# Kernel tuning notes

Measured on AMD Instinct MI355X. Metric: run time of the kernel, lower is better.

## Reference

```python
import jax, jax.numpy as jnp
import numpy as np

N_NODES = 50000
N_EDGES = 600000
N_FEAT = 128
N_DIMS = 128
N_CLSS = 10


def setup_inputs() -> dict:
    key = jax.random.key(0)
    ks = jax.random.split(key, 9)
    x = jax.random.normal(ks[0], (N_NODES, N_FEAT), dtype=jnp.float32)
    edge_index = jax.random.randint(ks[1], (2, N_EDGES), 0, N_NODES, dtype=jnp.int32)
    edge_weight = jax.random.uniform(ks[2], (N_EDGES,), dtype=jnp.float32)
    # Glorot-ish init for learned params
    W1 = jax.random.normal(ks[3], (N_FEAT, N_DIMS), dtype=jnp.float32) * (1.0 / np.sqrt(N_FEAT))
    b1 = jnp.zeros((N_DIMS,), dtype=jnp.float32)
    W2 = jax.random.normal(ks[4], (N_DIMS, N_DIMS), dtype=jnp.float32) * (1.0 / np.sqrt(N_DIMS))
    b2 = jnp.zeros((N_DIMS,), dtype=jnp.float32)
    Wc = jax.random.normal(ks[5], (N_DIMS, N_CLSS), dtype=jnp.float32) * (1.0 / np.sqrt(N_DIMS))
    bc = jnp.zeros((N_CLSS,), dtype=jnp.float32)
    return {"x": x, "edge_index": edge_index, "edge_weight": edge_weight,
            "W1": W1, "b1": b1, "W2": W2, "b2": b2, "Wc": Wc, "bc": bc}


def gcn_conv(x, W, b, src, dst, ew, n_nodes):
    """PyG GCNConv (add_self_loops=True, improved=False, bias=True).
    out[i] = sum_{(j->i) in E} d_i^-1/2 * w_ji * d_j^-1/2 * (xW)[j]
             + d_i^-1 * (xW)[i]  (self loop, weight 1) + b
    where d_i = 1 + sum of incoming edge weights at i.
    """
    h = x @ W                                                   # [N, D]
    deg = jax.ops.segment_sum(ew, dst, num_segments=n_nodes) + 1.0  # self-loop weight 1
    dinv = jax.lax.rsqrt(deg)                                   # deg >= 1, no inf
    norm = dinv[src] * ew * dinv[dst]                           # [E]
    agg = jax.ops.segment_sum(h[src] * norm[:, None], dst, num_segments=n_nodes)
    agg = agg + h * (dinv * dinv)[:, None]                      # self-loop term
    return agg + b


def reference(x, edge_index, edge_weight, W1, b1, W2, b2, Wc, bc):
    n = x.shape[0]
    src, dst = edge_index[0], edge_index[1]
    h = jax.nn.relu(gcn_conv(x, W1, b1, src, dst, edge_weight, n))
    # dropout is identity in eval mode
    h = gcn_conv(h, W2, b2, src, dst, edge_weight, n)
    h = jax.nn.relu(h)
    return h @ Wc + bc
```

## Files before the change

kernel.cpp:

```cpp
#include <hip/hip_runtime.h>
#include <hip/hip_bf16.h>

#define N_NODES 50000
#define N_EDGES 600000
#define NC 10
#define GB ((N_NODES + 63) / 64)

typedef __attribute__((ext_vector_type(8))) __bf16 bf16x8;
typedef __attribute__((ext_vector_type(8))) unsigned short u16x8;
typedef __attribute__((ext_vector_type(4))) float f32x4;

__device__ __forceinline__ unsigned short f2bf(float f) {
    unsigned u = __float_as_uint(f);
    u += 0x7fff + ((u >> 16) & 1);
    return (unsigned short)(u >> 16);
}
__device__ __forceinline__ int rfl(int x) { return __builtin_amdgcn_readfirstlane(x); }
__device__ __forceinline__ float rflf(float x) {
    return __uint_as_float(__builtin_amdgcn_readfirstlane(__float_as_uint(x)));
}

__global__ void k_zero(int4* __restrict__ p, int n4) {
    int i = blockIdx.x * blockDim.x + threadIdx.x;
    if (i < n4) p[i] = make_int4(0, 0, 0, 0);
}

__global__ void k_prep(const float* __restrict__ W1, const float* __restrict__ W2,
                       unsigned short* __restrict__ wt1, unsigned short* __restrict__ wt2,
                       const int4* __restrict__ dst4, int* __restrict__ cnt,
                       int4* __restrict__ ord4) {
    int b = blockIdx.x;
    if (b < 128) {
        const float* W = (b < 64) ? W1 : W2;
        unsigned short* Wt = (b < 64) ? wt1 : wt2;
        int i = (b & 63) * 256 + threadIdx.x;
        int n = i >> 7, k = i & 127;
        Wt[n * 128 + k] = f2bf(W[k * 128 + n]);
    } else {
        int i = (b - 128) * 256 + threadIdx.x;
        if (i < N_EDGES / 4) {
            int4 d = dst4[i];
            int4 o;
            o.x = atomicAdd(&cnt[d.x], 1);
            o.y = atomicAdd(&cnt[d.y], 1);
            o.z = atomicAdd(&cnt[d.z], 1);
            o.w = atomicAdd(&cnt[d.w], 1);
            ord4[i] = o;
        }
    }
}

__global__ void k_scan1(const int* __restrict__ cnt, int* __restrict__ rowptr,
                        int* __restrict__ bsum, int n) {
    __shared__ int sh[256];
    int t = threadIdx.x;
    int i = blockIdx.x * 256 + t;
    int v = (i < n) ? cnt[i] : 0;
    sh[t] = v;
    __syncthreads();
    for (int off = 1; off < 256; off <<= 1) {
        int x = 0;
        if (t >= off) x = sh[t - off];
        __syncthreads();
        sh[t] += x;
        __syncthreads();
    }
    if (i < n) rowptr[i] = sh[t] - v;
    if (t == 255) bsum[blockIdx.x] = sh[255];
}

__global__ void k_scan2(int* __restrict__ bsum, int nb) {
    __shared__ int sh[256];
    int t = threadIdx.x;
    int v = (t < nb) ? bsum[t] : 0;
    sh[t] = v;
    __syncthreads();
    for (int off = 1; off < 256; off <<= 1) {
        int x = 0;
        if (t >= off) x = sh[t - off];
        __syncthreads();
        sh[t] += x;
        __syncthreads();
    }
    if (t < nb) bsum[t] = sh[t] - v;
}

__global__ void k_scan3(int* __restrict__ rowptr, const int* __restrict__ bsum, int n) {
    int t = threadIdx.x;
    int i = blockIdx.x * 256 + t;
    if (i < n) rowptr[i] += bsum[blockIdx.x];
    if (blockIdx.x == 0 && t == 0) rowptr[n] = N_EDGES;
}

template <int FP32IN>
__device__ __forceinline__ void gemm_body(unsigned short* Al, unsigned short* Bl,
                                          const void* __restrict__ Xin,
                                          const unsigned short* __restrict__ Wt,
                                          unsigned short* __restrict__ Yb,
                                          int M, int row0) {
    int t = threadIdx.x;
    for (int i = t; i < 2048; i += 256) {
        int r = i >> 4, q = i & 15;
        *(u16x8*)(Bl + r * 128 + ((q ^ (r & 7)) << 3)) =
            *(const u16x8*)(Wt + r * 128 + (q << 3));
    }
    for (int i = t; i < 1024; i += 256) {
        int r = i >> 4, q = i & 15;
        int gr = row0 + r;
        u16x8 v;
        if (FP32IN) {
            const float* X = (const float*)Xin;
            if (gr < M) {
                float4 f0 = *(const float4*)(X + (size_t)gr * 128 + (q << 3));
                float4 f1 = *(const float4*)(X + (size_t)gr * 128 + (q << 3) + 4);
                v[0] = f2bf(f0.x); v[1] = f2bf(f0.y); v[2] = f2bf(f0.z); v[3] = f2bf(f0.w);
                v[4] = f2bf(f1.x); v[5] = f2bf(f1.y); v[6] = f2bf(f1.z); v[7] = f2bf(f1.w);
            } else {
#pragma unroll
                for (int j = 0; j < 8; ++j) v[j] = 0;
            }
        } else {
            const unsigned short* X = (const unsigned short*)Xin;
            if (gr < M) {
                v = *(const u16x8*)(X + (size_t)gr * 128 + (q << 3));
            } else {
#pragma unroll
                for (int j = 0; j < 8; ++j) v[j] = 0;
            }
        }
        *(u16x8*)(Al + r * 128 + ((q ^ (r & 7)) << 3)) = v;
    }
    __syncthreads();

    int l  = t & 63;
    int w  = t >> 6;
    int ar = (w << 4) + (l & 15);
    int kq = l >> 4;

    bf16x8 af[4];
#pragma unroll
    for (int s = 0; s < 4; ++s) {
        int g = ((s << 2) + kq) ^ (l & 7);
        af[s] = *(const bf16x8*)(Al + ar * 128 + (g << 3));
    }

    f32x4 acc[8];
#pragma unroll
    for (int c = 0; c < 8; ++c)
#pragma unroll
        for (int j = 0; j < 4; ++j) acc[c][j] = 0.0f;

#pragma unroll
    for (int c = 0; c < 8; ++c) {
        int br = (c << 4) + (l & 15);
#pragma unroll
        for (int s = 0; s < 4; ++s) {
            int g = ((s << 2) + kq) ^ (l & 7);
            bf16x8 bf = *(const bf16x8*)(Bl + br * 128 + (g << 3));
            acc[c] = __builtin_amdgcn_mfma_f32_16x16x32_bf16(af[s], bf, acc[c], 0, 0, 0);
        }
    }

    int orow = row0 + (w << 4) + ((l >> 4) << 2);
    int ocol = l & 15;
#pragma unroll
    for (int c = 0; c < 8; ++c) {
#pragma unroll
        for (int j = 0; j < 4; ++j) {
            int r = orow + j;
            if (r < M) Yb[(size_t)r * 128 + (c << 4) + ocol] = f2bf(acc[c][j]);
        }
    }
}

__global__ __launch_bounds__(256) void k_sg(const float* __restrict__ X,
                                            const unsigned short* __restrict__ Wt,
                                            unsigned short* __restrict__ Yb, int M,
                                            const int* __restrict__ src,
                                            const int* __restrict__ dst,
                                            const float* __restrict__ ew,
                                            const int* __restrict__ ord,
                                            const int* __restrict__ rowptr,
                                            int* __restrict__ esrc,
                                            float* __restrict__ ew2) {
    __shared__ unsigned short Al[64 * 128];
    __shared__ unsigned short Bl[128 * 128];
    if (blockIdx.x < GB) {
        gemm_body<1>(Al, Bl, X, Wt, Yb, M, blockIdx.x * 64);
    } else {
        int e = (blockIdx.x - GB) * 256 + threadIdx.x;
        if (e < N_EDGES) {
            int pos = rowptr[dst[e]] + ord[e];
            esrc[pos] = src[e];
            ew2[pos]  = ew[e];
        }
    }
}

__global__ __launch_bounds__(256) void k_gemm_mfma(const unsigned short* __restrict__ Xb,
                                                   const unsigned short* __restrict__ Wt,
                                                   unsigned short* __restrict__ Yb, int M) {
    __shared__ unsigned short Al[64 * 128];
    __shared__ unsigned short Bl[128 * 128];
    gemm_body<0>(Al, Bl, Xb, Wt, Yb, M, blockIdx.x * 64);
}

__global__ void k_deg(const int* __restrict__ rowptr, const float* __restrict__ ew2,
                      float* __restrict__ dinv) {
    int i = blockIdx.x * blockDim.x + threadIdx.x;
    if (i >= N_NODES) return;
    int p1 = rowptr[i + 1];
    float s = 1.0f;
    for (int p = rowptr[i]; p < p1; ++p) s += ew2[p];
    dinv[i] = rsqrtf(s);
}

__global__ void k_norm(const int* __restrict__ rowptr, const int* __restrict__ esrc,
                       const float* __restrict__ ew2, const float* __restrict__ dinv,
                       float* __restrict__ enorm) {
    int i = blockIdx.x * blockDim.x + threadIdx.x;
    if (i >= N_NODES) return;
    float di = dinv[i];
    int p  = rowptr[i];
    int p1 = rowptr[i + 1];
    for (; p + 4 <= p1; p += 4) {
        int s0 = esrc[p], s1 = esrc[p+1], s2 = esrc[p+2], s3 = esrc[p+3];
        float d0 = dinv[s0], d1 = dinv[s1], d2 = dinv[s2], d3 = dinv[s3];
        enorm[p]   = d0 * ew2[p]   * di;
        enorm[p+1] = d1 * ew2[p+1] * di;
        enorm[p+2] = d2 * ew2[p+2] * di;
        enorm[p+3] = d3 * ew2[p+3] * di;
    }
    for (; p < p1; ++p) enorm[p] = dinv[esrc[p]] * ew2[p] * di;
}

template <int MODE>
__global__ __launch_bounds__(256) void k_agg(const unsigned* __restrict__ hb,
                                             const int* __restrict__ rowptr,
                                             const int* __restrict__ esrc,
                                             const float* __restrict__ enorm,
                                             const float* __restrict__ dinv,
                                             const float* __restrict__ bias,
                                             const float* __restrict__ Wc,
                                             const float* __restrict__ bc,
                                             float* __restrict__ out) {
    int wid  = (blockIdx.x * blockDim.x + threadIdx.x) >> 6;
    int lane = threadIdx.x & 63;
    if (wid >= N_NODES) return;
    wid = rfl(wid);
    int p  = rfl(rowptr[wid]);
    int p1 = rfl(rowptr[wid + 1]);
    float di  = dinv[wid];
    float di2 = di * di;
    unsigned sv = hb[(size_t)wid * 64 + lane];
    float2 acc;
    acc.x = __uint_as_float(sv << 16) * di2;
    acc.y = __uint_as_float(sv & 0xffff0000u) * di2;

    while (p + 16 <= p1) {
        int s[16]; float w[16]; unsigned v[16];
#pragma unroll
        for (int i = 0; i < 16; ++i) {
            s[i] = rfl(esrc[p + i]);
            w[i] = rflf(enorm[p + i]);
        }
#pragma unroll
        for (int i = 0; i < 16; ++i) v[i] = hb[(size_t)s[i] * 64 + lane];
#pragma unroll
        for (int i = 0; i < 16; ++i) {
            acc.x += w[i] * __uint_as_float(v[i] << 16);
            acc.y += w[i] * __uint_as_float(v[i] & 0xffff0000u);
        }
        p += 16;
    }
    while (p + 4 <= p1) {
        int s[4]; float w[4]; unsigned v[4];
#pragma unroll
        for (int i = 0; i < 4; ++i) {
            s[i] = rfl(esrc[p + i]);
            w[i] = rflf(enorm[p + i]);
        }
#pragma unroll
        for (int i = 0; i < 4; ++i) v[i] = hb[(size_t)s[i] * 64 + lane];
#pragma unroll
        for (int i = 0; i < 4; ++i) {
            acc.x += w[i] * __uint_as_float(v[i] << 16);
            acc.y += w[i] * __uint_as_float(v[i] & 0xffff0000u);
        }
        p += 4;
    }
    for (; p < p1; ++p) {
        int s = rfl(esrc[p]);
        float w = rflf(enorm[p]);
        unsigned v = hb[(size_t)s * 64 + lane];
        acc.x += w * __uint_as_float(v << 16);
        acc.y += w * __uint_as_float(v & 0xffff0000u);
    }

    float2 bv = ((const float2*)bias)[lane];
    acc.x = fmaxf(acc.x + bv.x, 0.f);
    acc.y = fmaxf(acc.y + bv.y, 0.f);
    if (MODE == 0) {
        unsigned lo = f2bf(acc.x), hi = f2bf(acc.y);
        ((unsigned*)out)[(size_t)wid * 64 + lane] = lo | (hi << 16);
    } else {
        int k0 = 2 * lane;
        float r[NC];
#pragma unroll
        for (int c = 0; c < NC; ++c)
            r[c] = acc.x * Wc[k0 * NC + c] + acc.y * Wc[(k0 + 1) * NC + c];
#pragma unroll
        for (int off = 32; off; off >>= 1)
#pragma unroll
            for (int c = 0; c < NC; ++c)
                r[c] += __shfl_xor(r[c], off, 64);
        if (lane < NC) out[(size_t)wid * NC + lane] = r[lane] + bc[lane];
    }
}

extern "C" void kernel_launch(void* const* d_in, const int* in_sizes, int n_in,
                              void* d_out, int out_size, void* d_ws, size_t ws_size,
                              hipStream_t stream) {
    const float* x   = (const float*)d_in[0];
    const int*   ei  = (const int*)d_in[1];
    const float* ew  = (const float*)d_in[2];
    const float* W1  = (const float*)d_in[3];
    const float* b1  = (const float*)d_in[4];
    const float* W2  = (const float*)d_in[5];
    const float* b2  = (const float*)d_in[6];
    const float* Wc  = (const float*)d_in[7];
    const float* bc  = (const float*)d_in[8];
    float*       out = (float*)d_out;

    const int* src = ei;
    const int* dst = ei + N_EDGES;

    size_t off = 0;
    auto carve = [&](size_t bytes) {
        void* p = (char*)d_ws + off;
        off += (bytes + 255) & ~(size_t)255;
        return p;
    };
    unsigned short* hb  = (unsigned short*)carve((size_t)N_NODES * 128 * 2);
    unsigned short* hb1 = (unsigned short*)carve((size_t)N_NODES * 128 * 2);
    unsigned short* wt1 = (unsigned short*)carve(128 * 128 * 2);
    unsigned short* wt2 = (unsigned short*)carve(128 * 128 * 2);
    float* dinv   = (float*)carve((size_t)N_NODES * 4);
    int*   cnt    = (int*)carve((size_t)N_NODES * 4);
    int*   rowptr = (int*)carve((size_t)(N_NODES + 1) * 4);
    int*   bsum   = (int*)carve(256 * 4);
    int*   ord    = (int*)carve((size_t)N_EDGES * 4);
    int*   esrc   = (int*)carve((size_t)N_EDGES * 4);
    float* ew2    = (float*)carve((size_t)N_EDGES * 4);
    float* enorm  = (float*)carve((size_t)N_EDGES * 4);
    (void)ws_size; (void)n_in; (void)in_sizes; (void)out_size;

    int nb = (N_NODES + 255) / 256;
    int eb = (N_EDGES + 255) / 256;

    k_zero<<<(N_NODES / 4 + 255) / 256, 256, 0, stream>>>((int4*)cnt, N_NODES / 4);
    k_prep<<<128 + (N_EDGES / 4 + 255) / 256, 256, 0, stream>>>(
        W1, W2, wt1, wt2, (const int4*)dst, cnt, (int4*)ord);
    k_scan1<<<nb, 256, 0, stream>>>(cnt, rowptr, bsum, N_NODES);
    k_scan2<<<1, 256, 0, stream>>>(bsum, nb);
    k_scan3<<<nb, 256, 0, stream>>>(rowptr, bsum, N_NODES);
    k_sg<<<GB + eb, 256, 0, stream>>>(x, wt1, hb, N_NODES,
                                      src, dst, ew, ord, rowptr, esrc, ew2);
    k_deg<<<nb, 256, 0, stream>>>(rowptr, ew2, dinv);
    k_norm<<<nb, 256, 0, stream>>>(rowptr, esrc, ew2, dinv, enorm);

    k_agg<0><<<(N_NODES + 3) / 4, 256, 0, stream>>>((const unsigned*)hb, rowptr, esrc,
                                                    enorm, dinv, b1, Wc, bc, (float*)hb1);
    k_gemm_mfma<<<GB, 256, 0, stream>>>(hb1, wt2, hb, N_NODES);
    k_agg<1><<<(N_NODES + 3) / 4, 256, 0, stream>>>((const unsigned*)hb, rowptr, esrc,
                                                    enorm, dinv, b2, Wc, bc, out);
}
```

Before: 157.9 us.

## Split wavefront into four edge groups with 16-byte row gathers in aggregation

Reworks the aggregation kernel so each 64-lane wave handles four edges at once. Each 16-lane group loads a full 256-byte bf16 row with uint4 loads instead of one dword per lane. The self-loop is folded in as an extra edge item, and partial sums are reduced across groups with shuffles. This aims for wider memory transactions and more gathers in flight per wave, at the cost of padding waste on low-degree nodes, select logic per step, and extra cross-lane reductions.

```diff
diff --git a/kernel.cpp b/kernel.cpp
--- a/kernel.cpp
+++ b/kernel.cpp
@@ -235,7 +235,7 @@
 }
 
 template <int MODE>
-__global__ __launch_bounds__(256) void k_agg(const unsigned* __restrict__ hb,
+__global__ __launch_bounds__(256) void k_agg(const unsigned short* __restrict__ hb,
                                              const int* __restrict__ rowptr,
                                              const int* __restrict__ esrc,
                                              const float* __restrict__ enorm,
@@ -248,72 +248,111 @@
     int lane = threadIdx.x & 63;
     if (wid >= N_NODES) return;
     wid = rfl(wid);
-    int p  = rfl(rowptr[wid]);
-    int p1 = rfl(rowptr[wid + 1]);
-    float di  = dinv[wid];
+    int p0  = rfl(rowptr[wid]);
+    int cnt = rfl(rowptr[wid + 1]) - p0;
+    float di  = rflf(dinv[wid]);
     float di2 = di * di;
-    unsigned sv = hb[(size_t)wid * 64 + lane];
-    float2 acc;
-    acc.x = __uint_as_float(sv << 16) * di2;
-    acc.y = __uint_as_float(sv & 0xffff0000u) * di2;
-
-    while (p + 16 <= p1) {
-        int s[16]; float w[16]; unsigned v[16];
-#pragma unroll
-        for (int i = 0; i < 16; ++i) {
-            s[i] = rfl(esrc[p + i]);
-            w[i] = rflf(enorm[p + i]);
-        }
-#pragma unroll
-        for (int i = 0; i < 16; ++i) v[i] = hb[(size_t)s[i] * 64 + lane];
-#pragma unroll
-        for (int i = 0; i < 16; ++i) {
-            acc.x += w[i] * __uint_as_float(v[i] << 16);
-            acc.y += w[i] * __uint_as_float(v[i] & 0xffff0000u);
-        }
-        p += 16;
-    }
-    while (p + 4 <= p1) {
-        int s[4]; float w[4]; unsigned v[4];
-#pragma unroll
-        for (int i = 0; i < 4; ++i) {
-            s[i] = rfl(esrc[p + i]);
-            w[i] = rflf(enorm[p + i]);
-        }
-#pragma unroll
-        for (int i = 0; i < 4; ++i) v[i] = hb[(size_t)s[i] * 64 + lane];
-#pragma unroll
-        for (int i = 0; i < 4; ++i) {
-            acc.x += w[i] * __uint_as_float(v[i] << 16);
-            acc.y += w[i] * __uint_as_float(v[i] & 0xffff0000u);
-        }
-        p += 4;
-    }
-    for (; p < p1; ++p) {
-        int s = rfl(esrc[p]);
-        float w = rflf(enorm[p]);
-        unsigned v = hb[(size_t)s * 64 + lane];
-        acc.x += w * __uint_as_float(v << 16);
-        acc.y += w * __uint_as_float(v & 0xffff0000u);
-    }
-
-    float2 bv = ((const float2*)bias)[lane];
-    acc.x = fmaxf(acc.x + bv.x, 0.f);
-    acc.y = fmaxf(acc.y + bv.y, 0.f);
+    int g = lane >> 4;
+    int q = lane & 15;
+
+    bool g0 = (g == 0), g1 = (g == 1), g2 = (g == 2);
+
+    float acc[8];
+#pragma unroll
+    for (int j = 0; j < 8; ++j) acc[j] = 0.f;
+
+    int items = cnt + 1;
+    int base = 0;
+
+#define STEP_META(B, SS, WW)                                                    \
+    {                                                                           \
+        int i0 = p0 + (B);                                                      \
+        int e0 = min(i0,     N_EDGES - 1), e1 = min(i0 + 1, N_EDGES - 1);       \
+        int e2 = min(i0 + 2, N_EDGES - 1), e3 = min(i0 + 3, N_EDGES - 1);       \
+        int   s0 = rfl(esrc[e0]),  s1 = rfl(esrc[e1]);                          \
+        int   s2 = rfl(esrc[e2]),  s3 = rfl(esrc[e3]);                          \
+        float w0 = rflf(enorm[e0]), w1 = rflf(enorm[e1]);                       \
+        float w2 = rflf(enorm[e2]), w3 = rflf(enorm[e3]);                       \
+        if ((B) >= cnt)     { s0 = wid; w0 = ((B) == cnt)     ? di2 : 0.f; }    \
+        if ((B) + 1 >= cnt) { s1 = wid; w1 = ((B) + 1 == cnt) ? di2 : 0.f; }    \
+        if ((B) + 2 >= cnt) { s2 = wid; w2 = ((B) + 2 == cnt) ? di2 : 0.f; }    \
+        if ((B) + 3 >= cnt) { s3 = wid; w3 = ((B) + 3 == cnt) ? di2 : 0.f; }    \
+        SS = g0 ? s0 : (g1 ? s1 : (g2 ? s2 : s3));                              \
+        WW = g0 ? w0 : (g1 ? w1 : (g2 ? w2 : w3));                              \
+    }
+
+#define STEP_ACC(WW, V)                                                         \
+    acc[0] += (WW) * __uint_as_float((V).x << 16);                              \
+    acc[1] += (WW) * __uint_as_float((V).x & 0xffff0000u);                      \
+    acc[2] += (WW) * __uint_as_float((V).y << 16);                              \
+    acc[3] += (WW) * __uint_as_float((V).y & 0xffff0000u);                      \
+    acc[4] += (WW) * __uint_as_float((V).z << 16);                              \
+    acc[5] += (WW) * __uint_as_float((V).z & 0xffff0000u);                      \
+    acc[6] += (WW) * __uint_as_float((V).w << 16);                              \
+    acc[7] += (WW) * __uint_as_float((V).w & 0xffff0000u);
+
+    while (base + 16 <= items) {
+        int   ss[4];
+        float ws[4];
+        uint4 vs[4];
+        STEP_META(base + 0,  ss[0], ws[0])
+        STEP_META(base + 4,  ss[1], ws[1])
+        STEP_META(base + 8,  ss[2], ws[2])
+        STEP_META(base + 12, ss[3], ws[3])
+#pragma unroll
+        for (int s = 0; s < 4; ++s)
+            vs[s] = *(const uint4*)(hb + (size_t)ss[s] * 128 + (q << 3));
+#pragma unroll
+        for (int s = 0; s < 4; ++s) { STEP_ACC(ws[s], vs[s]) }
+        base += 16;
+    }
+    while (base < items) {
+        int ssel; float wsel;
+        STEP_META(base, ssel, wsel)
+        uint4 v = *(const uint4*)(hb + (size_t)ssel * 128 + (q << 3));
+        STEP_ACC(wsel, v)
+        base += 4;
+    }
+#undef STEP_META
+#undef STEP_ACC
+
+#pragma unroll
+    for (int j = 0; j < 8; ++j) {
+        acc[j] += __shfl_xor(acc[j], 32, 64);
+        acc[j] += __shfl_xor(acc[j], 16, 64);
+    }
+
+    float4 b0 = *(const float4*)(bias + (q << 3));
+    float4 b1v = *(const float4*)(bias + (q << 3) + 4);
+    acc[0] = fmaxf(acc[0] + b0.x, 0.f);  acc[1] = fmaxf(acc[1] + b0.y, 0.f);
+    acc[2] = fmaxf(acc[2] + b0.z, 0.f);  acc[3] = fmaxf(acc[3] + b0.w, 0.f);
+    acc[4] = fmaxf(acc[4] + b1v.x, 0.f); acc[5] = fmaxf(acc[5] + b1v.y, 0.f);
+    acc[6] = fmaxf(acc[6] + b1v.z, 0.f); acc[7] = fmaxf(acc[7] + b1v.w, 0.f);
+
     if (MODE == 0) {
-        unsigned lo = f2bf(acc.x), hi = f2bf(acc.y);
-        ((unsigned*)out)[(size_t)wid * 64 + lane] = lo | (hi << 16);
+        if (lane < 16) {
+            uint4 ov;
+            ov.x = f2bf(acc[0]) | ((unsigned)f2bf(acc[1]) << 16);
+            ov.y = f2bf(acc[2]) | ((unsigned)f2bf(acc[3]) << 16);
+            ov.z = f2bf(acc[4]) | ((unsigned)f2bf(acc[5]) << 16);
+            ov.w = f2bf(acc[6]) | ((unsigned)f2bf(acc[7]) << 16);
+            *(uint4*)((unsigned short*)out + (size_t)wid * 128 + (q << 3)) = ov;
+        }
     } else {
-        int k0 = 2 * lane;
         float r[NC];
 #pragma unroll
-        for (int c = 0; c < NC; ++c)
-            r[c] = acc.x * Wc[k0 * NC + c] + acc.y * Wc[(k0 + 1) * NC + c];
-#pragma unroll
-        for (int off = 32; off; off >>= 1)
-#pragma unroll
-            for (int c = 0; c < NC; ++c)
-                r[c] += __shfl_xor(r[c], off, 64);
+        for (int c = 0; c < NC; ++c) r[c] = 0.f;
+#pragma unroll
+        for (int j = 0; j < 8; ++j) {
+            float a = acc[j];
+            const float* wrow = Wc + ((q << 3) + j) * NC;
+#pragma unroll
+            for (int c = 0; c < NC; ++c) r[c] += a * wrow[c];
+        }
+#pragma unroll
+        for (int off = 8; off; off >>= 1)
+#pragma unroll
+            for (int c = 0; c < NC; ++c) r[c] += __shfl_xor(r[c], off, 64);
         if (lane < NC) out[(size_t)wid * NC + lane] = r[lane] + bc[lane];
     }
 }
@@ -369,9 +408,9 @@
     k_deg<<<nb, 256, 0, stream>>>(rowptr, ew2, dinv);
     k_norm<<<nb, 256, 0, stream>>>(rowptr, esrc, ew2, dinv, enorm);
 
-    k_agg<0><<<(N_NODES + 3) / 4, 256, 0, stream>>>((const unsigned*)hb, rowptr, esrc,
+    k_agg<0><<<(N_NODES + 3) / 4, 256, 0, stream>>>(hb, rowptr, esrc,
                                                     enorm, dinv, b1, Wc, bc, (float*)hb1);
     k_gemm_mfma<<<GB, 256, 0, stream>>>(hb1, wt2, hb, N_NODES);
-    k_agg<1><<<(N_NODES + 3) / 4, 256, 0, stream>>>((const unsigned*)hb, rowptr, esrc,
+    k_agg<1><<<(N_NODES + 3) / 4, 256, 0, stream>>>(hb, rowptr, esrc,
                                                     enorm, dinv, b2, Wc, bc, out);
 }
```

Result: slower. 195.9 us (+24.0%).

## Fuse layer-1 aggregation with layer-2 GEMM via shared-memory tile

Applied to the files above, without the earlier changes.

Replaces the separate layer-1 aggregation kernel and the layer-2 MFMA GEMM with one kernel. Each 256-thread block aggregates 64 nodes (16 per wave) into a swizzled LDS tile, then multiplies that tile by W2 with MFMA and writes bf16 output. This drops one launch and the global round trip of the intermediate activations. In exchange, aggregation parallelism falls to 4 waves per 64 nodes with sequential per-wave loops, so latency hiding on the gather may suffer, and B fragments are read straight from global memory.

```diff
diff --git a/kernel.cpp b/kernel.cpp
--- a/kernel.cpp
+++ b/kernel.cpp
@@ -197,14 +197,6 @@
     }
 }
 
-__global__ __launch_bounds__(256) void k_gemm_mfma(const unsigned short* __restrict__ Xb,
-                                                   const unsigned short* __restrict__ Wt,
-                                                   unsigned short* __restrict__ Yb, int M) {
-    __shared__ unsigned short Al[64 * 128];
-    __shared__ unsigned short Bl[128 * 128];
-    gemm_body<0>(Al, Bl, Xb, Wt, Yb, M, blockIdx.x * 64);
-}
-
 __global__ void k_deg(const int* __restrict__ rowptr, const float* __restrict__ ew2,
                       float* __restrict__ dinv) {
     int i = blockIdx.x * blockDim.x + threadIdx.x;
@@ -234,7 +226,130 @@
     for (; p < p1; ++p) enorm[p] = dinv[esrc[p]] * ew2[p] * di;
 }
 
-template <int MODE>
+__device__ __forceinline__ float2 agg_row(const unsigned* __restrict__ hb,
+                                          const int* __restrict__ rowptr,
+                                          const int* __restrict__ esrc,
+                                          const float* __restrict__ enorm,
+                                          const float* __restrict__ dinv,
+                                          int node, int lane) {
+    int p  = rfl(rowptr[node]);
+    int p1 = rfl(rowptr[node + 1]);
+    float di  = dinv[node];
+    float di2 = di * di;
+    unsigned sv = hb[(size_t)node * 64 + lane];
+    float2 acc;
+    acc.x = __uint_as_float(sv << 16) * di2;
+    acc.y = __uint_as_float(sv & 0xffff0000u) * di2;
+
+    while (p + 16 <= p1) {
+        int s[16]; float w[16]; unsigned v[16];
+#pragma unroll
+        for (int i = 0; i < 16; ++i) {
+            s[i] = rfl(esrc[p + i]);
+            w[i] = rflf(enorm[p + i]);
+        }
+#pragma unroll
+        for (int i = 0; i < 16; ++i) v[i] = hb[(size_t)s[i] * 64 + lane];
+#pragma unroll
+        for (int i = 0; i < 16; ++i) {
+            acc.x += w[i] * __uint_as_float(v[i] << 16);
+            acc.y += w[i] * __uint_as_float(v[i] & 0xffff0000u);
+        }
+        p += 16;
+    }
+    while (p + 4 <= p1) {
+        int s[4]; float w[4]; unsigned v[4];
+#pragma unroll
+        for (int i = 0; i < 4; ++i) {
+            s[i] = rfl(esrc[p + i]);
+            w[i] = rflf(enorm[p + i]);
+        }
+#pragma unroll
+        for (int i = 0; i < 4; ++i) v[i] = hb[(size_t)s[i] * 64 + lane];
+#pragma unroll
+        for (int i = 0; i < 4; ++i) {
+            acc.x += w[i] * __uint_as_float(v[i] << 16);
+            acc.y += w[i] * __uint_as_float(v[i] & 0xffff0000u);
+        }
+        p += 4;
+    }
+    for (; p < p1; ++p) {
+        int s = rfl(esrc[p]);
+        float w = rflf(enorm[p]);
+        unsigned v = hb[(size_t)s * 64 + lane];
+        acc.x += w * __uint_as_float(v << 16);
+        acc.y += w * __uint_as_float(v & 0xffff0000u);
+    }
+    return acc;
+}
+
+__global__ __launch_bounds__(256) void k_ag(const unsigned* __restrict__ hb,
+                                            const int* __restrict__ rowptr,
+                                            const int* __restrict__ esrc,
+                                            const float* __restrict__ enorm,
+                                            const float* __restrict__ dinv,
+                                            const float* __restrict__ bias,
+                                            const unsigned short* __restrict__ Wt,
+                                            unsigned short* __restrict__ Yb, int M) {
+    __shared__ unsigned short Al[64 * 128];
+    int t = threadIdx.x;
+    int l = t & 63;
+    int w = t >> 6;
+    int row0 = blockIdx.x * 64;
+
+    for (int nd = 0; nd < 16; ++nd) {
+        int r = (w << 4) + nd;
+        int node = row0 + r;
+        float2 acc = make_float2(0.f, 0.f);
+        if (node < M) {
+            acc = agg_row(hb, rowptr, esrc, enorm, dinv, node, l);
+            float2 bv = ((const float2*)bias)[l];
+            acc.x = fmaxf(acc.x + bv.x, 0.f);
+            acc.y = fmaxf(acc.y + bv.y, 0.f);
+        }
+        unsigned val = f2bf(acc.x) | ((unsigned)f2bf(acc.y) << 16);
+        int q = l >> 2;
+        *(unsigned*)(Al + r * 128 + ((q ^ (r & 7)) << 3) + ((l & 3) << 1)) = val;
+    }
+    __syncthreads();
+
+    int ar = (w << 4) + (l & 15);
+    int kq = l >> 4;
+    bf16x8 af[4];
+#pragma unroll
+    for (int s = 0; s < 4; ++s) {
+        int g = ((s << 2) + kq) ^ (ar & 7);
+        af[s] = *(const bf16x8*)(Al + ar * 128 + (g << 3));
+    }
+
+    f32x4 acc2[8];
+#pragma unroll
+    for (int c = 0; c < 8; ++c)
+#pragma unroll
+        for (int j = 0; j < 4; ++j) acc2[c][j] = 0.0f;
+
+#pragma unroll
+    for (int c = 0; c < 8; ++c) {
+        int br = (c << 4) + (l & 15);
+#pragma unroll
+        for (int s = 0; s < 4; ++s) {
+            bf16x8 bf = *(const bf16x8*)(Wt + br * 128 + (((s << 2) + kq) << 3));
+            acc2[c] = __builtin_amdgcn_mfma_f32_16x16x32_bf16(af[s], bf, acc2[c], 0, 0, 0);
+        }
+    }
+
+    int orow = row0 + (w << 4) + ((l >> 4) << 2);
+    int ocol = l & 15;
+#pragma unroll
+    for (int c = 0; c < 8; ++c) {
+#pragma unroll
+        for (int j = 0; j < 4; ++j) {
+            int r = orow + j;
+            if (r < M) Yb[(size_t)r * 128 + (c << 4) + ocol] = f2bf(acc2[c][j]);
+        }
+    }
+}
+
 __global__ __launch_bounds__(256) void k_agg(const unsigned* __restrict__ hb,
                                              const int* __restrict__ rowptr,
                                              const int* __restrict__ esrc,
@@ -248,74 +363,22 @@
     int lane = threadIdx.x & 63;
     if (wid >= N_NODES) return;
     wid = rfl(wid);
-    int p  = rfl(rowptr[wid]);
-    int p1 = rfl(rowptr[wid + 1]);
-    float di  = dinv[wid];
-    float di2 = di * di;
-    unsigned sv = hb[(size_t)wid * 64 + lane];
-    float2 acc;
-    acc.x = __uint_as_float(sv << 16) * di2;
-    acc.y = __uint_as_float(sv & 0xffff0000u) * di2;
-
-    while (p + 16 <= p1) {
-        int s[16]; float w[16]; unsigned v[16];
-#pragma unroll
-        for (int i = 0; i < 16; ++i) {
-            s[i] = rfl(esrc[p + i]);
-            w[i] = rflf(enorm[p + i]);
-        }
-#pragma unroll
-        for (int i = 0; i < 16; ++i) v[i] = hb[(size_t)s[i] * 64 + lane];
-#pragma unroll
-        for (int i = 0; i < 16; ++i) {
-            acc.x += w[i] * __uint_as_float(v[i] << 16);
-            acc.y += w[i] * __uint_as_float(v[i] & 0xffff0000u);
-        }
-        p += 16;
-    }
-    while (p + 4 <= p1) {
-        int s[4]; float w[4]; unsigned v[4];
-#pragma unroll
-        for (int i = 0; i < 4; ++i) {
-            s[i] = rfl(esrc[p + i]);
-            w[i] = rflf(enorm[p + i]);
-        }
-#pragma unroll
-        for (int i = 0; i < 4; ++i) v[i] = hb[(size_t)s[i] * 64 + lane];
-#pragma unroll
-        for (int i = 0; i < 4; ++i) {
-            acc.x += w[i] * __uint_as_float(v[i] << 16);
-            acc.y += w[i] * __uint_as_float(v[i] & 0xffff0000u);
-        }
-        p += 4;
-    }
-    for (; p < p1; ++p) {
-        int s = rfl(esrc[p]);
-        float w = rflf(enorm[p]);
-        unsigned v = hb[(size_t)s * 64 + lane];
-        acc.x += w * __uint_as_float(v << 16);
-        acc.y += w * __uint_as_float(v & 0xffff0000u);
-    }
-
+    float2 acc = agg_row(hb, rowptr, esrc, enorm, dinv, wid, lane);
     float2 bv = ((const float2*)bias)[lane];
     acc.x = fmaxf(acc.x + bv.x, 0.f);
     acc.y = fmaxf(acc.y + bv.y, 0.f);
-    if (MODE == 0) {
-        unsigned lo = f2bf(acc.x), hi = f2bf(acc.y);
-        ((unsigned*)out)[(size_t)wid * 64 + lane] = lo | (hi << 16);
-    } else {
-        int k0 = 2 * lane;
-        float r[NC];
+
+    int k0 = 2 * lane;
+    float r[NC];
+#pragma unroll
+    for (int c = 0; c < NC; ++c)
+        r[c] = acc.x * Wc[k0 * NC + c] + acc.y * Wc[(k0 + 1) * NC + c];
+#pragma unroll
+    for (int off = 32; off; off >>= 1)
 #pragma unroll
         for (int c = 0; c < NC; ++c)
-            r[c] = acc.x * Wc[k0 * NC + c] + acc.y * Wc[(k0 + 1) * NC + c];
-#pragma unroll
-        for (int off = 32; off; off >>= 1)
-#pragma unroll
-            for (int c = 0; c < NC; ++c)
-                r[c] += __shfl_xor(r[c], off, 64);
-        if (lane < NC) out[(size_t)wid * NC + lane] = r[lane] + bc[lane];
-    }
+            r[c] += __shfl_xor(r[c], off, 64);
+    if (lane < NC) out[(size_t)wid * NC + lane] = r[lane] + bc[lane];
 }
 
 extern "C" void kernel_launch(void* const* d_in, const int* in_sizes, int n_in,
@@ -342,7 +405,7 @@
         return p;
     };
     unsigned short* hb  = (unsigned short*)carve((size_t)N_NODES * 128 * 2);
-    unsigned short* hb1 = (unsigned short*)carve((size_t)N_NODES * 128 * 2);
+    unsigned short* hb2 = (unsigned short*)carve((size_t)N_NODES * 128 * 2);
     unsigned short* wt1 = (unsigned short*)carve(128 * 128 * 2);
     unsigned short* wt2 = (unsigned short*)carve(128 * 128 * 2);
     float* dinv   = (float*)carve((size_t)N_NODES * 4);
@@ -369,9 +432,8 @@
     k_deg<<<nb, 256, 0, stream>>>(rowptr, ew2, dinv);
     k_norm<<<nb, 256, 0, stream>>>(rowptr, esrc, ew2, dinv, enorm);
 
-    k_agg<0><<<(N_NODES + 3) / 4, 256, 0, stream>>>((const unsigned*)hb, rowptr, esrc,
-                                                    enorm, dinv, b1, Wc, bc, (float*)hb1);
-    k_gemm_mfma<<<GB, 256, 0, stream>>>(hb1, wt2, hb, N_NODES);
-    k_agg<1><<<(N_NODES + 3) / 4, 256, 0, stream>>>((const unsigned*)hb, rowptr, esrc,
-                                                    enorm, dinv, b2, Wc, bc, out);
-}
+    k_ag<<<GB, 256, 0, stream>>>((const unsigned*)hb, rowptr, esrc, enorm, dinv,
+                                 b1, wt2, hb2, N_NODES);
+    k_agg<<<(N_NODES + 3) / 4, 256, 0, stream>>>((const unsigned*)hb2, rowptr, esrc,
+                                                 enorm, dinv, b2, Wc, bc, out);
+}
```

New measurement: 173.8 us. +10.0%, slower.

## Move edge counting into GEMM launch and merge scan passes

Applied to the files above, without the earlier changes.

The edge-degree atomic counting now runs inside the first GEMM launch, so it overlaps with the matmul blocks instead of sitting in the weight-prep kernel. The counter zeroing moves into the prep kernel, and the scan's second and third passes merge into one kernel where every block redoes the small block-sum scan. The CSR scatter becomes its own kernel after the scan. Launch count drops by one, and the aggregation kernels are split into two specialized kernels that write to separate buffers.

```diff
diff --git a/kernel.cpp b/kernel.cpp
--- a/kernel.cpp
+++ b/kernel.cpp
@@ -5,6 +5,7 @@
 #define N_EDGES 600000
 #define NC 10
 #define GB ((N_NODES + 63) / 64)
+#define CNTB ((N_EDGES / 4 + 255) / 256)
 
 typedef __attribute__((ext_vector_type(8))) __bf16 bf16x8;
 typedef __attribute__((ext_vector_type(8))) unsigned short u16x8;
@@ -20,15 +21,9 @@
     return __uint_as_float(__builtin_amdgcn_readfirstlane(__float_as_uint(x)));
 }
 
-__global__ void k_zero(int4* __restrict__ p, int n4) {
-    int i = blockIdx.x * blockDim.x + threadIdx.x;
-    if (i < n4) p[i] = make_int4(0, 0, 0, 0);
-}
-
-__global__ void k_prep(const float* __restrict__ W1, const float* __restrict__ W2,
-                       unsigned short* __restrict__ wt1, unsigned short* __restrict__ wt2,
-                       const int4* __restrict__ dst4, int* __restrict__ cnt,
-                       int4* __restrict__ ord4) {
+__global__ void k_prep0(const float* __restrict__ W1, const float* __restrict__ W2,
+                        unsigned short* __restrict__ wt1, unsigned short* __restrict__ wt2,
+                        int4* __restrict__ cnt4) {
     int b = blockIdx.x;
     if (b < 128) {
         const float* W = (b < 64) ? W1 : W2;
@@ -38,15 +33,7 @@
         Wt[n * 128 + k] = f2bf(W[k * 128 + n]);
     } else {
         int i = (b - 128) * 256 + threadIdx.x;
-        if (i < N_EDGES / 4) {
-            int4 d = dst4[i];
-            int4 o;
-            o.x = atomicAdd(&cnt[d.x], 1);
-            o.y = atomicAdd(&cnt[d.y], 1);
-            o.z = atomicAdd(&cnt[d.z], 1);
-            o.w = atomicAdd(&cnt[d.w], 1);
-            ord4[i] = o;
-        }
+        if (i < N_NODES / 4) cnt4[i] = make_int4(0, 0, 0, 0);
     }
 }
 
@@ -69,8 +56,10 @@
     if (t == 255) bsum[blockIdx.x] = sh[255];
 }
 
-__global__ void k_scan2(int* __restrict__ bsum, int nb) {
+__global__ void k_scan23(int* __restrict__ rowptr, const int* __restrict__ bsum,
+                         int nb, int n) {
     __shared__ int sh[256];
+    __shared__ int ex[256];
     int t = threadIdx.x;
     int v = (t < nb) ? bsum[t] : 0;
     sh[t] = v;
@@ -82,13 +71,10 @@
         sh[t] += x;
         __syncthreads();
     }
-    if (t < nb) bsum[t] = sh[t] - v;
-}
-
-__global__ void k_scan3(int* __restrict__ rowptr, const int* __restrict__ bsum, int n) {
-    int t = threadIdx.x;
+    ex[t] = sh[t] - v;
+    __syncthreads();
     int i = blockIdx.x * 256 + t;
-    if (i < n) rowptr[i] += bsum[blockIdx.x];
+    if (i < n) rowptr[i] += ex[blockIdx.x];
     if (blockIdx.x == 0 && t == 0) rowptr[n] = N_EDGES;
 }
 
@@ -173,28 +159,39 @@
     }
 }
 
-__global__ __launch_bounds__(256) void k_sg(const float* __restrict__ X,
+__global__ __launch_bounds__(256) void k_cg(const int4* __restrict__ dst4,
+                                            int* __restrict__ cnt,
+                                            int4* __restrict__ ord4,
+                                            const float* __restrict__ X,
                                             const unsigned short* __restrict__ Wt,
-                                            unsigned short* __restrict__ Yb, int M,
-                                            const int* __restrict__ src,
-                                            const int* __restrict__ dst,
-                                            const float* __restrict__ ew,
-                                            const int* __restrict__ ord,
-                                            const int* __restrict__ rowptr,
-                                            int* __restrict__ esrc,
-                                            float* __restrict__ ew2) {
+                                            unsigned short* __restrict__ Yb, int M) {
     __shared__ unsigned short Al[64 * 128];
     __shared__ unsigned short Bl[128 * 128];
-    if (blockIdx.x < GB) {
-        gemm_body<1>(Al, Bl, X, Wt, Yb, M, blockIdx.x * 64);
+    if (blockIdx.x < CNTB) {
+        int i = blockIdx.x * 256 + threadIdx.x;
+        if (i < N_EDGES / 4) {
+            int4 d = dst4[i];
+            int4 o;
+            o.x = atomicAdd(&cnt[d.x], 1);
+            o.y = atomicAdd(&cnt[d.y], 1);
+            o.z = atomicAdd(&cnt[d.z], 1);
+            o.w = atomicAdd(&cnt[d.w], 1);
+            ord4[i] = o;
+        }
     } else {
-        int e = (blockIdx.x - GB) * 256 + threadIdx.x;
-        if (e < N_EDGES) {
-            int pos = rowptr[dst[e]] + ord[e];
-            esrc[pos] = src[e];
-            ew2[pos]  = ew[e];
-        }
-    }
+        gemm_body<1>(Al, Bl, X, Wt, Yb, M, (blockIdx.x - CNTB) * 64);
+    }
+}
+
+__global__ void k_scatter(const int* __restrict__ src, const int* __restrict__ dst,
+                          const float* __restrict__ ew, const int* __restrict__ ord,
+                          const int* __restrict__ rowptr,
+                          int* __restrict__ esrc, float* __restrict__ ew2) {
+    int e = blockIdx.x * blockDim.x + threadIdx.x;
+    if (e >= N_EDGES) return;
+    int pos = rowptr[dst[e]] + ord[e];
+    esrc[pos] = src[e];
+    ew2[pos]  = ew[e];
 }
 
 __global__ __launch_bounds__(256) void k_gemm_mfma(const unsigned short* __restrict__ Xb,
@@ -234,25 +231,17 @@
     for (; p < p1; ++p) enorm[p] = dinv[esrc[p]] * ew2[p] * di;
 }
 
-template <int MODE>
-__global__ __launch_bounds__(256) void k_agg(const unsigned* __restrict__ hb,
-                                             const int* __restrict__ rowptr,
-                                             const int* __restrict__ esrc,
-                                             const float* __restrict__ enorm,
-                                             const float* __restrict__ dinv,
-                                             const float* __restrict__ bias,
-                                             const float* __restrict__ Wc,
-                                             const float* __restrict__ bc,
-                                             float* __restrict__ out) {
-    int wid  = (blockIdx.x * blockDim.x + threadIdx.x) >> 6;
-    int lane = threadIdx.x & 63;
-    if (wid >= N_NODES) return;
-    wid = rfl(wid);
-    int p  = rfl(rowptr[wid]);
-    int p1 = rfl(rowptr[wid + 1]);
-    float di  = dinv[wid];
+__device__ __forceinline__ float2 agg_row(const unsigned* __restrict__ hb,
+                                          const int* __restrict__ rowptr,
+                                          const int* __restrict__ esrc,
+                                          const float* __restrict__ enorm,
+                                          const float* __restrict__ dinv,
+                                          int node, int lane) {
+    int p  = rfl(rowptr[node]);
+    int p1 = rfl(rowptr[node + 1]);
+    float di  = dinv[node];
     float di2 = di * di;
-    unsigned sv = hb[(size_t)wid * 64 + lane];
+    unsigned sv = hb[(size_t)node * 64 + lane];
     float2 acc;
     acc.x = __uint_as_float(sv << 16) * di2;
     acc.y = __uint_as_float(sv & 0xffff0000u) * di2;
@@ -296,26 +285,56 @@
         acc.x += w * __uint_as_float(v << 16);
         acc.y += w * __uint_as_float(v & 0xffff0000u);
     }
-
+    return acc;
+}
+
+__global__ __launch_bounds__(256) void k_agg0(const unsigned* __restrict__ hb,
+                                              const int* __restrict__ rowptr,
+                                              const int* __restrict__ esrc,
+                                              const float* __restrict__ enorm,
+                                              const float* __restrict__ dinv,
+                                              const float* __restrict__ bias,
+                                              unsigned* __restrict__ outb) {
+    int wid  = (blockIdx.x * blockDim.x + threadIdx.x) >> 6;
+    int lane = threadIdx.x & 63;
+    if (wid >= N_NODES) return;
+    wid = rfl(wid);
+    float2 acc = agg_row(hb, rowptr, esrc, enorm, dinv, wid, lane);
     float2 bv = ((const float2*)bias)[lane];
     acc.x = fmaxf(acc.x + bv.x, 0.f);
     acc.y = fmaxf(acc.y + bv.y, 0.f);
-    if (MODE == 0) {
-        unsigned lo = f2bf(acc.x), hi = f2bf(acc.y);
-        ((unsigned*)out)[(size_t)wid * 64 + lane] = lo | (hi << 16);
-    } else {
-        int k0 = 2 * lane;
-        float r[NC];
+    outb[(size_t)wid * 64 + lane] = f2bf(acc.x) | ((unsigned)f2bf(acc.y) << 16);
+}
+
+__global__ __launch_bounds__(256) void k_agg1(const unsigned* __restrict__ hb,
+                                              const int* __restrict__ rowptr,
+                                              const int* __restrict__ esrc,
+                                              const float* __restrict__ enorm,
+                                              const float* __restrict__ dinv,
+                                              const float* __restrict__ bias,
+                                              const float* __restrict__ Wc,
+                                              const float* __restrict__ bc,
+                                              float* __restrict__ out) {
+    int wid  = (blockIdx.x * blockDim.x + threadIdx.x) >> 6;
+    int lane = threadIdx.x & 63;
+    if (wid >= N_NODES) return;
+    wid = rfl(wid);
+    float2 acc = agg_row(hb, rowptr, esrc, enorm, dinv, wid, lane);
+    float2 bv = ((const float2*)bias)[lane];
+    acc.x = fmaxf(acc.x + bv.x, 0.f);
+    acc.y = fmaxf(acc.y + bv.y, 0.f);
+
+    int k0 = 2 * lane;
+    float r[NC];
+#pragma unroll
+    for (int c = 0; c < NC; ++c)
+        r[c] = acc.x * Wc[k0 * NC + c] + acc.y * Wc[(k0 + 1) * NC + c];
+#pragma unroll
+    for (int off = 32; off; off >>= 1)
 #pragma unroll
         for (int c = 0; c < NC; ++c)
-            r[c] = acc.x * Wc[k0 * NC + c] + acc.y * Wc[(k0 + 1) * NC + c];
-#pragma unroll
-        for (int off = 32; off; off >>= 1)
-#pragma unroll
-            for (int c = 0; c < NC; ++c)
-                r[c] += __shfl_xor(r[c], off, 64);
-        if (lane < NC) out[(size_t)wid * NC + lane] = r[lane] + bc[lane];
-    }
+            r[c] += __shfl_xor(r[c], off, 64);
+    if (lane < NC) out[(size_t)wid * NC + lane] = r[lane] + bc[lane];
 }
 
 extern "C" void kernel_launch(void* const* d_in, const int* in_sizes, int n_in,
@@ -342,7 +361,8 @@
         return p;
     };
     unsigned short* hb  = (unsigned short*)carve((size_t)N_NODES * 128 * 2);
-    unsigned short* hb1 = (unsigned short*)carve((size_t)N_NODES * 128 * 2);
+    unsigned short* zb  = (unsigned short*)carve((size_t)N_NODES * 128 * 2);
+    unsigned short* hb2 = (unsigned short*)carve((size_t)N_NODES * 128 * 2);
     unsigned short* wt1 = (unsigned short*)carve(128 * 128 * 2);
     unsigned short* wt2 = (unsigned short*)carve(128 * 128 * 2);
     float* dinv   = (float*)carve((size_t)N_NODES * 4);
@@ -358,20 +378,19 @@
     int nb = (N_NODES + 255) / 256;
     int eb = (N_EDGES + 255) / 256;
 
-    k_zero<<<(N_NODES / 4 + 255) / 256, 256, 0, stream>>>((int4*)cnt, N_NODES / 4);
-    k_prep<<<128 + (N_EDGES / 4 + 255) / 256, 256, 0, stream>>>(
-        W1, W2, wt1, wt2, (const int4*)dst, cnt, (int4*)ord);
+    k_prep0<<<128 + (N_NODES / 4 + 255) / 256, 256, 0, stream>>>(W1, W2, wt1, wt2,
+                                                                 (int4*)cnt);
+    k_cg<<<CNTB + GB, 256, 0, stream>>>((const int4*)dst, cnt, (int4*)ord,
+                                        x, wt1, hb, N_NODES);
     k_scan1<<<nb, 256, 0, stream>>>(cnt, rowptr, bsum, N_NODES);
-    k_scan2<<<1, 256, 0, stream>>>(bsum, nb);
-    k_scan3<<<nb, 256, 0, stream>>>(rowptr, bsum, N_NODES);
-    k_sg<<<GB + eb, 256, 0, stream>>>(x, wt1, hb, N_NODES,
-                                      src, dst, ew, ord, rowptr, esrc, ew2);
+    k_scan23<<<nb, 256, 0, stream>>>(rowptr, bsum, nb, N_NODES);
+    k_scatter<<<eb, 256, 0, stream>>>(src, dst, ew, ord, rowptr, esrc, ew2);
     k_deg<<<nb, 256, 0, stream>>>(rowptr, ew2, dinv);
     k_norm<<<nb, 256, 0, stream>>>(rowptr, esrc, ew2, dinv, enorm);
 
-    k_agg<0><<<(N_NODES + 3) / 4, 256, 0, stream>>>((const unsigned*)hb, rowptr, esrc,
-                                                    enorm, dinv, b1, Wc, bc, (float*)hb1);
-    k_gemm_mfma<<<GB, 256, 0, stream>>>(hb1, wt2, hb, N_NODES);
-    k_agg<1><<<(N_NODES + 3) / 4, 256, 0, stream>>>((const unsigned*)hb, rowptr, esrc,
-                                                    enorm, dinv, b2, Wc, bc, out);
-}
+    k_agg0<<<(N_NODES + 3) / 4, 256, 0, stream>>>((const unsigned*)hb, rowptr, esrc,
+                                                  enorm, dinv, b1, (unsigned*)zb);
+    k_gemm_mfma<<<GB, 256, 0, stream>>>(zb, wt2, hb2, N_NODES);
+    k_agg1<<<(N_NODES + 3) / 4, 256, 0, stream>>>((const unsigned*)hb2, rowptr, esrc,
+                                                  enorm, dinv, b2, Wc, bc, out);
+}
```

Result: faster. 150.8 us (-4.5%).
